# Kernel optimization log

Hardware: AMD Instinct MI355X
Metric: run time of the kernel (lower is better)

The kernel has to match this reference:

```python
import jax, jax.numpy as jnp
import numpy as np

N_NODES = 100000


def _gcn_norm(edge_index, num_nodes):
    # Add self-loops, then symmetric normalization D^-1/2 A D^-1/2 (PyG gcn_norm).
    loops = jnp.arange(num_nodes, dtype=edge_index.dtype)
    src = jnp.concatenate([edge_index[0], loops])
    dst = jnp.concatenate([edge_index[1], loops])
    ew = jnp.ones(src.shape[0], dtype=jnp.float32)
    deg = jax.ops.segment_sum(ew, dst, num_segments=num_nodes)
    dinv = jnp.where(deg > 0, jax.lax.rsqrt(deg), 0.0)
    norm = dinv[src] * ew * dinv[dst]
    return src, dst, norm


def _prop_gcn_conv(x, W, b, src, dst, norm, num_nodes, prop_nums):
    # PropGCNConv: linear transform once, then prop_nums hops of normalized
    # sparse propagation (gather from src, scale, scatter-add to dst), + bias.
    x = x @ W
    for _ in range(prop_nums):
        msgs = x[src] * norm[:, None]              # [E, d]
        x = jax.ops.segment_sum(msgs, dst, num_segments=num_nodes)
    return x + b


def setup_inputs() -> dict:
    key = jax.random.key(0)
    k1, k2, k3, k4 = jax.random.split(key, 4)
    in_dim, hid_dim, num_classes = 128, 64, 40
    n_edges = 800000
    x = jax.random.normal(k1, (N_NODES, in_dim), dtype=jnp.float32)
    W0 = jax.random.normal(k2, (in_dim, hid_dim), dtype=jnp.float32) * (1.0 / np.sqrt(in_dim))
    b0 = jnp.zeros((hid_dim,), dtype=jnp.float32)
    Wc = jax.random.normal(k3, (hid_dim, num_classes), dtype=jnp.float32) * (1.0 / np.sqrt(hid_dim))
    bc = jnp.zeros((num_classes,), dtype=jnp.float32)
    edge_index = jax.random.randint(k4, (2, n_edges), 0, N_NODES, dtype=jnp.int64)
    return {"x": x, "W0": W0, "b0": b0, "Wc": Wc, "bc": bc,
            "edge_index": edge_index, "prop_nums": 30}


def reference(x, W0, b0, Wc, bc, edge_index, prop_nums):
    n = x.shape[0]
    src, dst, norm = _gcn_norm(edge_index, n)
    # feat_bottleneck: conv -> relu -> dropout (eval mode -> identity)
    h = _prop_gcn_conv(x, W0, b0, src, dst, norm, n, prop_nums)
    h = jax.nn.relu(h)
    # feat_classifier: single-hop PropGCNConv
    out = _prop_gcn_conv(h, Wc, bc, src, dst, norm, n, 1)
    return out
```

## Files before the change

### kernel.cpp

```cpp
#include <hip/hip_runtime.h>

#define NN  100000
#define NE  800000
#define NNZ 900000
#define IN_DIM 128
#define HID 64
#define NC  40
#define HOPS 30

typedef _Float16 half8 __attribute__((ext_vector_type(8)));


__global__ void count_edges_k(const int* __restrict__ dst, int* __restrict__ cnt) {
    int e = blockIdx.x * blockDim.x + threadIdx.x;
    if (e < NE) atomicAdd(&cnt[dst[e]], 1);
}

__global__ void dinv_k(const int* __restrict__ cnt, float* __restrict__ dinv) {
    int i = blockIdx.x * blockDim.x + threadIdx.x;
    if (i < NN) dinv[i] = rsqrtf((float)(cnt[i] + 1));
}

__global__ void scan_blocks_k(const int* __restrict__ cnt, int* __restrict__ rp,
                              int* __restrict__ partials) {
    __shared__ int s[256];
    int tid = threadIdx.x;
    int i = blockIdx.x * 256 + tid;
    int v = (i < NN) ? (cnt[i] + 1) : 0;
    s[tid] = v;
    __syncthreads();
    for (int off = 1; off < 256; off <<= 1) {
        int t = (tid >= off) ? s[tid - off] : 0;
        __syncthreads();
        s[tid] += t;
        __syncthreads();
    }
    if (i < NN) rp[i] = s[tid] - v;
    if (tid == 255) partials[blockIdx.x] = s[255];
}

__global__ void scan_partials_k(int* __restrict__ partials, int nblk) {
    if (blockIdx.x == 0 && threadIdx.x == 0) {
        int acc = 0;
        for (int b = 0; b < nblk; ++b) { int t = partials[b]; partials[b] = acc; acc += t; }
    }
}

__global__ void add_offsets_k(int* __restrict__ rp, const int* __restrict__ partials) {
    int i = blockIdx.x * 256 + threadIdx.x;
    if (i < NN) rp[i] += partials[blockIdx.x];
    if (i == 0) rp[NN] = NNZ;
}

__global__ void fill_csr_k(const int* __restrict__ src, const int* __restrict__ dst,
                           const float* __restrict__ dinv, const int* __restrict__ rp,
                           int* __restrict__ cnt, int2* __restrict__ cv) {
    int e = blockIdx.x * blockDim.x + threadIdx.x;
    if (e >= NNZ) return;
    int pos;
    int2 p;
    if (e < NE) {
        int s = src[e], d = dst[e];
        int old = atomicAdd(&cnt[d], -1);
        pos = rp[d] + old - 1;
        p.x = s;
        p.y = __float_as_int(dinv[s] * dinv[d]);
    } else {
        int i = e - NE;
        pos = rp[i + 1] - 1;
        p.x = i;
        p.y = __float_as_int(dinv[i] * dinv[i]);
    }
    cv[pos] = p;
}


__global__ void __launch_bounds__(256, 2) gemm1_k(const float* __restrict__ x,
                                                  const float* __restrict__ W,
                                                  _Float16* __restrict__ out) {
    __shared__ float Ws[IN_DIM * HID];
    int t = threadIdx.x;
    for (int i = t; i < IN_DIM * HID / 4; i += 256)
        ((float4*)Ws)[i] = ((const float4*)W)[i];
    __syncthreads();
    int w = t >> 6, l = t & 63;
    int ch = w >> 1;
    int n0 = blockIdx.x * 256 + (w & 1) * 64 + l;
    int n1 = n0 + 128;
    int n0c = n0 < NN ? n0 : NN - 1;
    int n1c = n1 < NN ? n1 : NN - 1;
    const float4* xr0 = (const float4*)(x + (size_t)n0c * IN_DIM);
    const float4* xr1 = (const float4*)(x + (size_t)n1c * IN_DIM);
    float4 a0[8], a1[8];
#pragma unroll
    for (int c = 0; c < 8; ++c) {
        a0[c] = make_float4(0.f, 0.f, 0.f, 0.f);
        a1[c] = make_float4(0.f, 0.f, 0.f, 0.f);
    }
#pragma unroll 2
    for (int k4 = 0; k4 < IN_DIM / 4; ++k4) {
        float4 xv0 = xr0[k4];
        float4 xv1 = xr1[k4];
#pragma unroll
        for (int kk = 0; kk < 4; ++kk) {
            float xs0 = (kk == 0) ? xv0.x : (kk == 1) ? xv0.y : (kk == 2) ? xv0.z : xv0.w;
            float xs1 = (kk == 0) ? xv1.x : (kk == 1) ? xv1.y : (kk == 2) ? xv1.z : xv1.w;
            const float4* wr = (const float4*)(Ws + (k4 * 4 + kk) * HID + ch * 32);
#pragma unroll
            for (int c = 0; c < 8; ++c) {
                float4 wv = wr[c];
                a0[c].x = fmaf(xs0, wv.x, a0[c].x);
                a0[c].y = fmaf(xs0, wv.y, a0[c].y);
                a0[c].z = fmaf(xs0, wv.z, a0[c].z);
                a0[c].w = fmaf(xs0, wv.w, a0[c].w);
                a1[c].x = fmaf(xs1, wv.x, a1[c].x);
                a1[c].y = fmaf(xs1, wv.y, a1[c].y);
                a1[c].z = fmaf(xs1, wv.z, a1[c].z);
                a1[c].w = fmaf(xs1, wv.w, a1[c].w);
            }
        }
    }
    if (n0 < NN) {
        half8* o = (half8*)(out + (size_t)n0 * HID + ch * 32);
#pragma unroll
        for (int g = 0; g < 4; ++g) {
            half8 r;
            float4 lo = a0[g * 2], hi = a0[g * 2 + 1];
            r[0] = (_Float16)lo.x; r[1] = (_Float16)lo.y; r[2] = (_Float16)lo.z; r[3] = (_Float16)lo.w;
            r[4] = (_Float16)hi.x; r[5] = (_Float16)hi.y; r[6] = (_Float16)hi.z; r[7] = (_Float16)hi.w;
            o[g] = r;
        }
    }
    if (n1 < NN) {
        half8* o = (half8*)(out + (size_t)n1 * HID + ch * 32);
#pragma unroll
        for (int g = 0; g < 4; ++g) {
            half8 r;
            float4 lo = a1[g * 2], hi = a1[g * 2 + 1];
            r[0] = (_Float16)lo.x; r[1] = (_Float16)lo.y; r[2] = (_Float16)lo.z; r[3] = (_Float16)lo.w;
            r[4] = (_Float16)hi.x; r[5] = (_Float16)hi.y; r[6] = (_Float16)hi.z; r[7] = (_Float16)hi.w;
            o[g] = r;
        }
    }
}

__global__ void prop64_k(const _Float16* __restrict__ xin, _Float16* __restrict__ xout,
                         const int* __restrict__ rp, const int2* __restrict__ cv) {
    int wid  = threadIdx.x >> 6;
    int lane = threadIdx.x & 63;
    int n    = lane >> 5;
    int s    = (lane >> 3) & 3;
    int f    = lane & 7;
    int node = blockIdx.x * 8 + wid * 2 + n;
    int beg = rp[node], end = rp[node + 1];
    const half8* x8 = (const half8*)xin;
    float a0 = 0.f, a1 = 0.f, a2 = 0.f, a3 = 0.f, a4 = 0.f, a5 = 0.f, a6 = 0.f, a7 = 0.f;
    for (int e = beg + s; e < end; e += 16) {
        int  e1 = e + 4,  e2 = e + 8,  e3 = e + 12;
        bool p1 = e1 < end, p2 = e2 < end, p3 = e3 < end;
        int2 q0 = cv[e];
        int2 q1 = cv[p1 ? e1 : beg];
        int2 q2 = cv[p2 ? e2 : beg];
        int2 q3 = cv[p3 ? e3 : beg];
        float v0 = __int_as_float(q0.y);
        float v1 = p1 ? __int_as_float(q1.y) : 0.f;
        float v2 = p2 ? __int_as_float(q2.y) : 0.f;
        float v3 = p3 ? __int_as_float(q3.y) : 0.f;
        half8 x0 = x8[(size_t)q0.x * 8 + f];
        half8 x1 = x8[(size_t)q1.x * 8 + f];
        half8 x2 = x8[(size_t)q2.x * 8 + f];
        half8 x3 = x8[(size_t)q3.x * 8 + f];
        a0 += v0 * (float)x0[0] + v1 * (float)x1[0] + v2 * (float)x2[0] + v3 * (float)x3[0];
        a1 += v0 * (float)x0[1] + v1 * (float)x1[1] + v2 * (float)x2[1] + v3 * (float)x3[1];
        a2 += v0 * (float)x0[2] + v1 * (float)x1[2] + v2 * (float)x2[2] + v3 * (float)x3[2];
        a3 += v0 * (float)x0[3] + v1 * (float)x1[3] + v2 * (float)x2[3] + v3 * (float)x3[3];
        a4 += v0 * (float)x0[4] + v1 * (float)x1[4] + v2 * (float)x2[4] + v3 * (float)x3[4];
        a5 += v0 * (float)x0[5] + v1 * (float)x1[5] + v2 * (float)x2[5] + v3 * (float)x3[5];
        a6 += v0 * (float)x0[6] + v1 * (float)x1[6] + v2 * (float)x2[6] + v3 * (float)x3[6];
        a7 += v0 * (float)x0[7] + v1 * (float)x1[7] + v2 * (float)x2[7] + v3 * (float)x3[7];
    }
#pragma unroll
    for (int m = 8; m <= 16; m <<= 1) {
        a0 += __shfl_xor(a0, m); a1 += __shfl_xor(a1, m);
        a2 += __shfl_xor(a2, m); a3 += __shfl_xor(a3, m);
        a4 += __shfl_xor(a4, m); a5 += __shfl_xor(a5, m);
        a6 += __shfl_xor(a6, m); a7 += __shfl_xor(a7, m);
    }
    if (s == 0) {
        half8 r;
        r[0] = (_Float16)a0; r[1] = (_Float16)a1; r[2] = (_Float16)a2; r[3] = (_Float16)a3;
        r[4] = (_Float16)a4; r[5] = (_Float16)a5; r[6] = (_Float16)a6; r[7] = (_Float16)a7;
        ((half8*)xout)[(size_t)node * 8 + f] = r;
    }
}

__global__ void __launch_bounds__(256, 4) gemm2_k(const _Float16* __restrict__ h,
                                                  const float* __restrict__ b0,
                                                  const float* __restrict__ Wc,
                                                  _Float16* __restrict__ g) {
    __shared__ float Wcs[HID * NC];
    __shared__ float b0s[HID];
    int t = threadIdx.x;
    for (int i = t; i < HID * NC / 4; i += 256)
        ((float4*)Wcs)[i] = ((const float4*)Wc)[i];
    if (t < HID) b0s[t] = b0[t];
    __syncthreads();
    int node = blockIdx.x * 256 + t;
    if (node >= NN) return;
    const half8* hr = (const half8*)(h + (size_t)node * HID);
    float acc[NC];
#pragma unroll
    for (int c = 0; c < NC; ++c) acc[c] = 0.f;
#pragma unroll
    for (int j = 0; j < 8; ++j) {
        half8 hv = hr[j];
#pragma unroll
        for (int m = 0; m < 8; ++m) {
            int k = j * 8 + m;
            float fv = fmaxf((float)hv[m] + b0s[k], 0.f);
            const float4* wr = (const float4*)(Wcs + k * NC);
#pragma unroll
            for (int c4 = 0; c4 < NC / 4; ++c4) {
                float4 wv = wr[c4];
                acc[c4 * 4 + 0] = fmaf(fv, wv.x, acc[c4 * 4 + 0]);
                acc[c4 * 4 + 1] = fmaf(fv, wv.y, acc[c4 * 4 + 1]);
                acc[c4 * 4 + 2] = fmaf(fv, wv.z, acc[c4 * 4 + 2]);
                acc[c4 * 4 + 3] = fmaf(fv, wv.w, acc[c4 * 4 + 3]);
            }
        }
    }
    half8* go = (half8*)(g + (size_t)node * NC);
#pragma unroll
    for (int j = 0; j < 5; ++j) {
        half8 r;
#pragma unroll
        for (int m = 0; m < 8; ++m) r[m] = (_Float16)acc[j * 8 + m];
        go[j] = r;
    }
}

__global__ void prop40_k(const _Float16* __restrict__ g, float* __restrict__ out,
                         const int* __restrict__ rp, const int2* __restrict__ cv,
                         const float* __restrict__ bc) {
    int t = blockIdx.x * 256 + threadIdx.x;
    int node = t >> 6;
    int lane = threadIdx.x & 63;
    int s = lane >> 3;
    int f = lane & 7;
    int beg = rp[node], end = rp[node + 1];
    const half8* g8 = (const half8*)g;
    bool act = f < 5;
    float a0 = 0.f, a1 = 0.f, a2 = 0.f, a3 = 0.f, a4 = 0.f, a5 = 0.f, a6 = 0.f, a7 = 0.f;
    for (int e = beg + s; e < end; e += 16) {
        int  e1 = e + 8;
        bool p1 = e1 < end;
        int2 q0 = cv[e];
        int2 q1 = cv[p1 ? e1 : beg];
        float v0 = __int_as_float(q0.y);
        float v1 = p1 ? __int_as_float(q1.y) : 0.f;
        if (act) {
            half8 x0 = g8[(size_t)q0.x * 5 + f];
            half8 x1 = g8[(size_t)q1.x * 5 + f];
            a0 += v0 * (float)x0[0] + v1 * (float)x1[0];
            a1 += v0 * (float)x0[1] + v1 * (float)x1[1];
            a2 += v0 * (float)x0[2] + v1 * (float)x1[2];
            a3 += v0 * (float)x0[3] + v1 * (float)x1[3];
            a4 += v0 * (float)x0[4] + v1 * (float)x1[4];
            a5 += v0 * (float)x0[5] + v1 * (float)x1[5];
            a6 += v0 * (float)x0[6] + v1 * (float)x1[6];
            a7 += v0 * (float)x0[7] + v1 * (float)x1[7];
        }
    }
#pragma unroll
    for (int m = 8; m <= 32; m <<= 1) {
        a0 += __shfl_xor(a0, m); a1 += __shfl_xor(a1, m);
        a2 += __shfl_xor(a2, m); a3 += __shfl_xor(a3, m);
        a4 += __shfl_xor(a4, m); a5 += __shfl_xor(a5, m);
        a6 += __shfl_xor(a6, m); a7 += __shfl_xor(a7, m);
    }
    if (s == 0 && act) {
        float* o = out + (size_t)node * NC + f * 8;
        o[0] = a0 + bc[f * 8 + 0];
        o[1] = a1 + bc[f * 8 + 1];
        o[2] = a2 + bc[f * 8 + 2];
        o[3] = a3 + bc[f * 8 + 3];
        o[4] = a4 + bc[f * 8 + 4];
        o[5] = a5 + bc[f * 8 + 5];
        o[6] = a6 + bc[f * 8 + 6];
        o[7] = a7 + bc[f * 8 + 7];
    }
}


extern "C" void kernel_launch(void* const* d_in, const int* in_sizes, int n_in,
                              void* d_out, int out_size, void* d_ws, size_t ws_size,
                              hipStream_t stream) {
    const float* x  = (const float*)d_in[0];
    const float* W0 = (const float*)d_in[1];
    const float* b0 = (const float*)d_in[2];
    const float* Wc = (const float*)d_in[3];
    const float* bc = (const float*)d_in[4];
    const int*   ei = (const int*)d_in[5];
    const int* src = ei;
    const int* dst = ei + NE;

    char* ws = (char*)d_ws;
    size_t off = 0;
    auto alloc = [&](size_t bytes) -> void* {
        void* p = ws + off;
        off = (off + bytes + 255) & ~(size_t)255;
        return p;
    };
    float* dinv     = (float*)alloc((size_t)NN * 4);
    int*   rp       = (int*)  alloc((size_t)(NN + 1) * 4);
    int*   cnt      = (int*)  alloc((size_t)NN * 4);
    int*   partials = (int*)  alloc(512 * 4);
    int2*  cvp      = (int2*) alloc((size_t)NNZ * 8);
    _Float16* XA    = (_Float16*)alloc((size_t)NN * HID * 2);
    _Float16* XB    = (_Float16*)alloc((size_t)NN * HID * 2);
    _Float16* G     = (_Float16*)alloc((size_t)NN * NC * 2);

    const int nblk_n = (NN + 255) / 256;

    hipMemsetAsync(cnt, 0, (size_t)NN * 4, stream);
    count_edges_k<<<(NE + 255) / 256, 256, 0, stream>>>(dst, cnt);
    dinv_k       <<<nblk_n, 256, 0, stream>>>(cnt, dinv);
    scan_blocks_k<<<nblk_n, 256, 0, stream>>>(cnt, rp, partials);
    scan_partials_k<<<1, 64, 0, stream>>>(partials, nblk_n);
    add_offsets_k<<<nblk_n, 256, 0, stream>>>(rp, partials);
    fill_csr_k   <<<(NNZ + 255) / 256, 256, 0, stream>>>(src, dst, dinv, rp, cnt, cvp);

    gemm1_k<<<nblk_n, 256, 0, stream>>>(x, W0, XA);

    _Float16* a = XA;
    _Float16* b = XB;
    for (int hop = 0; hop < HOPS; ++hop) {
        prop64_k<<<NN / 8, 256, 0, stream>>>(a, b, rp, cvp);
        _Float16* tmp = a; a = b; b = tmp;
    }

    gemm2_k<<<nblk_n, 256, 0, stream>>>(a, b0, Wc, G);
    prop40_k<<<NN * HID / 256, 256, 0, stream>>>(G, (float*)d_out, rp, cvp, bc);
}
```

Before: 880.2 us.

## Parallelize partial-sum scan and restructure gemm1 to drop shared-memory weights

The single-thread serial scan over block partials becomes a 512-thread shared-memory Hillis-Steele scan. gemm1 no longer stages all of W in LDS. Each block now covers 64 nodes, and each wave computes a 16-column slice, reading W through wave-uniform loads (readfirstlane makes the column index scalar). This shrinks per-block LDS and registers, which should raise occupancy and block count, at the cost of more global/L1 traffic to W and more blocks each re-reading x rows.

```diff
diff --git a/kernel.cpp b/kernel.cpp
--- a/kernel.cpp
+++ b/kernel.cpp
@@ -40,10 +40,18 @@
 }
 
 __global__ void scan_partials_k(int* __restrict__ partials, int nblk) {
-    if (blockIdx.x == 0 && threadIdx.x == 0) {
-        int acc = 0;
-        for (int b = 0; b < nblk; ++b) { int t = partials[b]; partials[b] = acc; acc += t; }
-    }
+    __shared__ int s[512];
+    int tid = threadIdx.x;
+    int v = (tid < nblk) ? partials[tid] : 0;
+    s[tid] = v;
+    __syncthreads();
+    for (int off = 1; off < 512; off <<= 1) {
+        int t = (tid >= off) ? s[tid - off] : 0;
+        __syncthreads();
+        s[tid] += t;
+        __syncthreads();
+    }
+    if (tid < nblk) partials[tid] = s[tid] - v;
 }
 
 __global__ void add_offsets_k(int* __restrict__ rp, const int* __restrict__ partials) {
@@ -75,72 +83,45 @@
 }
 
 
-__global__ void __launch_bounds__(256, 2) gemm1_k(const float* __restrict__ x,
-                                                  const float* __restrict__ W,
-                                                  _Float16* __restrict__ out) {
-    __shared__ float Ws[IN_DIM * HID];
+__global__ void __launch_bounds__(256) gemm1_k(const float* __restrict__ x,
+                                               const float* __restrict__ W,
+                                               _Float16* __restrict__ out) {
     int t = threadIdx.x;
-    for (int i = t; i < IN_DIM * HID / 4; i += 256)
-        ((float4*)Ws)[i] = ((const float4*)W)[i];
-    __syncthreads();
-    int w = t >> 6, l = t & 63;
-    int ch = w >> 1;
-    int n0 = blockIdx.x * 256 + (w & 1) * 64 + l;
-    int n1 = n0 + 128;
-    int n0c = n0 < NN ? n0 : NN - 1;
-    int n1c = n1 < NN ? n1 : NN - 1;
-    const float4* xr0 = (const float4*)(x + (size_t)n0c * IN_DIM);
-    const float4* xr1 = (const float4*)(x + (size_t)n1c * IN_DIM);
-    float4 a0[8], a1[8];
-#pragma unroll
-    for (int c = 0; c < 8; ++c) {
-        a0[c] = make_float4(0.f, 0.f, 0.f, 0.f);
-        a1[c] = make_float4(0.f, 0.f, 0.f, 0.f);
-    }
-#pragma unroll 2
+    int cq = __builtin_amdgcn_readfirstlane(t >> 6);
+    int node = blockIdx.x * 64 + (t & 63);
+    int nc = node < NN ? node : NN - 1;
+    const float4* xr = (const float4*)(x + (size_t)nc * IN_DIM);
+    const float* Wq = W + cq * 16;
+    float acc[16];
+#pragma unroll
+    for (int c = 0; c < 16; ++c) acc[c] = 0.f;
+#pragma unroll 4
     for (int k4 = 0; k4 < IN_DIM / 4; ++k4) {
-        float4 xv0 = xr0[k4];
-        float4 xv1 = xr1[k4];
+        float4 xv = xr[k4];
 #pragma unroll
         for (int kk = 0; kk < 4; ++kk) {
-            float xs0 = (kk == 0) ? xv0.x : (kk == 1) ? xv0.y : (kk == 2) ? xv0.z : xv0.w;
-            float xs1 = (kk == 0) ? xv1.x : (kk == 1) ? xv1.y : (kk == 2) ? xv1.z : xv1.w;
-            const float4* wr = (const float4*)(Ws + (k4 * 4 + kk) * HID + ch * 32);
-#pragma unroll
-            for (int c = 0; c < 8; ++c) {
-                float4 wv = wr[c];
-                a0[c].x = fmaf(xs0, wv.x, a0[c].x);
-                a0[c].y = fmaf(xs0, wv.y, a0[c].y);
-                a0[c].z = fmaf(xs0, wv.z, a0[c].z);
-                a0[c].w = fmaf(xs0, wv.w, a0[c].w);
-                a1[c].x = fmaf(xs1, wv.x, a1[c].x);
-                a1[c].y = fmaf(xs1, wv.y, a1[c].y);
-                a1[c].z = fmaf(xs1, wv.z, a1[c].z);
-                a1[c].w = fmaf(xs1, wv.w, a1[c].w);
+            float xs = (kk == 0) ? xv.x : (kk == 1) ? xv.y : (kk == 2) ? xv.z : xv.w;
+            const float4* wr = (const float4*)(Wq + (k4 * 4 + kk) * HID);
+#pragma unroll
+            for (int c4 = 0; c4 < 4; ++c4) {
+                float4 wv = wr[c4];
+                acc[c4 * 4 + 0] = fmaf(xs, wv.x, acc[c4 * 4 + 0]);
+                acc[c4 * 4 + 1] = fmaf(xs, wv.y, acc[c4 * 4 + 1]);
+                acc[c4 * 4 + 2] = fmaf(xs, wv.z, acc[c4 * 4 + 2]);
+                acc[c4 * 4 + 3] = fmaf(xs, wv.w, acc[c4 * 4 + 3]);
             }
         }
     }
-    if (n0 < NN) {
-        half8* o = (half8*)(out + (size_t)n0 * HID + ch * 32);
-#pragma unroll
-        for (int g = 0; g < 4; ++g) {
-            half8 r;
-            float4 lo = a0[g * 2], hi = a0[g * 2 + 1];
-            r[0] = (_Float16)lo.x; r[1] = (_Float16)lo.y; r[2] = (_Float16)lo.z; r[3] = (_Float16)lo.w;
-            r[4] = (_Float16)hi.x; r[5] = (_Float16)hi.y; r[6] = (_Float16)hi.z; r[7] = (_Float16)hi.w;
-            o[g] = r;
+    if (node < NN) {
+        half8* o = (half8*)(out + (size_t)node * HID + cq * 16);
+        half8 r0, r1;
+#pragma unroll
+        for (int j = 0; j < 8; ++j) {
+            r0[j] = (_Float16)acc[j];
+            r1[j] = (_Float16)acc[j + 8];
         }
-    }
-    if (n1 < NN) {
-        half8* o = (half8*)(out + (size_t)n1 * HID + ch * 32);
-#pragma unroll
-        for (int g = 0; g < 4; ++g) {
-            half8 r;
-            float4 lo = a1[g * 2], hi = a1[g * 2 + 1];
-            r[0] = (_Float16)lo.x; r[1] = (_Float16)lo.y; r[2] = (_Float16)lo.z; r[3] = (_Float16)lo.w;
-            r[4] = (_Float16)hi.x; r[5] = (_Float16)hi.y; r[6] = (_Float16)hi.z; r[7] = (_Float16)hi.w;
-            o[g] = r;
-        }
+        o[0] = r0;
+        o[1] = r1;
     }
 }
 
@@ -326,11 +307,11 @@
     count_edges_k<<<(NE + 255) / 256, 256, 0, stream>>>(dst, cnt);
     dinv_k       <<<nblk_n, 256, 0, stream>>>(cnt, dinv);
     scan_blocks_k<<<nblk_n, 256, 0, stream>>>(cnt, rp, partials);
-    scan_partials_k<<<1, 64, 0, stream>>>(partials, nblk_n);
+    scan_partials_k<<<1, 512, 0, stream>>>(partials, nblk_n);
     add_offsets_k<<<nblk_n, 256, 0, stream>>>(rp, partials);
     fill_csr_k   <<<(NNZ + 255) / 256, 256, 0, stream>>>(src, dst, dinv, rp, cnt, cvp);
 
-    gemm1_k<<<nblk_n, 256, 0, stream>>>(x, W0, XA);
+    gemm1_k<<<(NN + 63) / 64, 256, 0, stream>>>(x, W0, XA);
 
     _Float16* a = XA;
     _Float16* b = XB;
```

Result: faster. 836.0 us (-5.0%).
